# Kernel optimization log

Hardware: AMD Instinct MI355X
Metric: run time of the kernel (lower is better)

## Reference

```python
import jax, jax.numpy as jnp
import numpy as np

B, S, V, D, DV = 8, 2048, 32000, 1024, 1152
NUM_IMG, PATCHES = 4, 576
IMG_POS = [100, 600, 1100, 1600]
IMAGE_TOKEN_ID = 31999


def setup_inputs() -> dict:
    key = jax.random.key(0)
    k1, k2, k3, k4 = jax.random.split(key, 4)
    texts = jax.random.randint(k1, (B, S), 0, 31000)
    texts = texts.at[:, jnp.array(IMG_POS)].set(IMAGE_TOKEN_ID)
    visual_features = jax.random.normal(k2, (B, NUM_IMG * PATCHES, DV), jnp.float32)
    embedding_table = jax.random.normal(k3, (V, D), jnp.float32) * 0.02
    W_proj = jax.random.normal(k4, (DV, D), jnp.float32) * 0.02
    b_proj = jnp.zeros((D,), jnp.float32)
    return {"visual_features": visual_features, "embedding_table": embedding_table,
            "W_proj": W_proj, "b_proj": b_proj, "texts": texts,
            "image_token_id": IMAGE_TOKEN_ID}


def _plan(texts_np, image_token_id, n_visual):
    # Host-side (int-only) plan: per-sample gather indices into [text_emb ; visual]
    # plus the nested block attention mask. Mirrors the torch ragged loops.
    Bn, Sn = texts_np.shape
    idx_list, cid_list, vis_list = [], [], []
    for b in range(Bn):
        pos = np.nonzero(texts_np[b] == image_token_id)[0]
        n = len(pos)
        if n == 0:
            idx_list.append(np.arange(Sn))
            cid_list.append(np.zeros(Sn, np.int64))
            vis_list.append(np.zeros(Sn, bool))
            continue
        per = n_visual // n
        text_chunks = []
        start = 0
        for p in pos:
            if p > start:
                text_chunks.append((start, int(p)))
                start = int(p) + 1
        if start < Sn:
            text_chunks.append((start, Sn))
        idx, cid, vis = [], [], []
        c = 0
        for i in range(n):
            if i < len(text_chunks):
                s, e = text_chunks[i]
                idx.append(np.arange(s, e)); cid.append(np.full(e - s, c)); vis.append(np.zeros(e - s, bool)); c += 1
            idx.append(Sn + np.arange(i * per, (i + 1) * per))
            cid.append(np.full(per, c)); vis.append(np.ones(per, bool)); c += 1
        if n < len(text_chunks):
            s, e = text_chunks[-1]
            idx.append(np.arange(s, e)); cid.append(np.full(e - s, c)); vis.append(np.zeros(e - s, bool))
        idx_list.append(np.concatenate(idx))
        cid_list.append(np.concatenate(cid))
        vis_list.append(np.concatenate(vis))
    L = max(len(x) for x in idx_list)
    idx_p = np.zeros((Bn, L), np.int64)
    valid = np.zeros((Bn, L), np.float32)
    mask = np.zeros((Bn, L, L), np.float32)
    for b in range(Bn):
        l = len(idx_list[b])
        idx_p[b, :l] = idx_list[b]
        valid[b, :l] = 1.0
        cid, vis = cid_list[b], vis_list[b]
        ar = np.arange(l)
        # block-causal: full attention to earlier chunks; within own chunk:
        # visual chunks bidirectional, text chunks causal
        m = (cid[None, :] < cid[:, None]) | (
            (cid[None, :] == cid[:, None]) & (vis[:, None] | (ar[None, :] <= ar[:, None])))
        mask[b, :l, :l] = m.astype(np.float32)
    return idx_p, valid, mask


def reference(visual_features, embedding_table, W_proj, b_proj, texts, image_token_id):
    texts_np = np.asarray(jax.device_get(texts))
    idx, valid, mask = _plan(texts_np, int(image_token_id), visual_features.shape[1])
    projected = visual_features @ W_proj + b_proj          # [B, Nv, D]
    text_emb = embedding_table[texts]                      # [B, S, D]
    combined = jnp.concatenate([text_emb, projected], axis=1)  # [B, S+Nv, D]
    fused = jnp.take_along_axis(combined, jnp.asarray(idx)[:, :, None], axis=1)
    fused = fused * jnp.asarray(valid)[:, :, None]
    return fused, jnp.asarray(mask)[:, None, :, :]
```

## Files before the change

### kernel.cpp

```cpp
#include <hip/hip_runtime.h>
#include <math.h>
#include <stdint.h>

#define MAXI 8
#define MAXSEG (2*MAXI+2)
#define VISBIT (1<<30)

typedef __attribute__((ext_vector_type(8))) short short8;
typedef __attribute__((ext_vector_type(4))) float f32x4;

static __device__ __forceinline__ unsigned short f2bf(float f) {
  union { float f; unsigned int u; } v; v.f = f;
  unsigned int x = v.u;
  unsigned int r = (x + 0x7FFFu + ((x >> 16) & 1u)) >> 16;
  return (unsigned short)r;
}

static __device__ __forceinline__ void gload_lds16(const void* g, void* lds) {
  __builtin_amdgcn_global_load_lds((const __attribute__((address_space(1))) void*)g,
                                   (__attribute__((address_space(3))) void*)lds, 16, 0, 0);
}

__global__ void plan_kernel(const int* __restrict__ texts, const int* __restrict__ imgtok_p,
                            int S, int n_visual, int L,
                            int* __restrict__ seg, int* __restrict__ nsegA, int* __restrict__ lenA,
                            int* __restrict__ perA, int* __restrict__ nimgA, int* __restrict__ ostA)
{
  int b = blockIdx.x;
  __shared__ int spos[256];
  __shared__ int scnt;
  if (threadIdx.x == 0) scnt = 0;
  __syncthreads();
  int tok = imgtok_p[0];
  for (int s = threadIdx.x; s < S; s += blockDim.x) {
    if (texts[(size_t)b*S + s] == tok) {
      int i = atomicAdd(&scnt, 1);
      if (i < 256) spos[i] = s;
    }
  }
  __syncthreads();
  if (threadIdx.x != 0) return;
  int n = scnt; if (n > MAXI) n = MAXI;
  for (int i = 1; i < n; i++) {
    int key = spos[i]; int j = i - 1;
    while (j >= 0 && spos[j] > key) { spos[j+1] = spos[j]; j--; }
    spos[j+1] = key;
  }
  int* sg = seg + b*MAXSEG*4;
  int ns = 0, o = 0, c = 0, per = 1;
  if (n == 0) {
    sg[0] = 0; sg[1] = 0; sg[2] = S; sg[3] = 0; ns = 1; o = S;
  } else {
    per = n_visual / n;
    int tcs[MAXI+1], tce[MAXI+1]; int ntc = 0; int start = 0;
    for (int i = 0; i < n; i++) {
      int p = spos[i];
      if (p > start) { tcs[ntc] = start; tce[ntc] = p; ntc++; }
      start = p + 1;
    }
    if (start < S) { tcs[ntc] = start; tce[ntc] = S; ntc++; }
    for (int i = 0; i < n; i++) {
      if (i < ntc) {
        sg[ns*4+0] = o; sg[ns*4+1] = tcs[i]; sg[ns*4+2] = tce[i]-tcs[i]; sg[ns*4+3] = (c<<1);
        o += tce[i]-tcs[i]; c++; ns++;
      }
      ostA[b*MAXI + i] = o;
      sg[ns*4+0] = o; sg[ns*4+1] = i*per; sg[ns*4+2] = per; sg[ns*4+3] = (c<<1)|1;
      o += per; c++; ns++;
    }
    if (n < ntc) {
      sg[ns*4+0] = o; sg[ns*4+1] = tcs[ntc-1]; sg[ns*4+2] = tce[ntc-1]-tcs[ntc-1]; sg[ns*4+3] = (c<<1);
      o += sg[ns*4+2]; ns++;
    }
  }
  nsegA[b] = ns; lenA[b] = o; perA[b] = per; nimgA[b] = n;
  for (int i = n; i < MAXI; i++) ostA[b*MAXI + i] = 0;
  for (int t = ns; t < MAXSEG; t++) { sg[t*4+0]=0; sg[t*4+1]=0; sg[t*4+2]=0; sg[t*4+3]=0; }
}

__global__ void fill_kernel(const int* __restrict__ texts, int S, int L, int bpb,
                            const int* __restrict__ seg, const int* __restrict__ nsegA,
                            int* __restrict__ srcA, int* __restrict__ cidvA)
{
  int b = blockIdx.x / bpb;
  int j = (blockIdx.x % bpb) * blockDim.x + threadIdx.x;
  if (j >= L) return;
  int ns = nsegA[b];
  const int* sg = seg + b*MAXSEG*4;
  int src = -1, cv = -1;
  for (int t = 0; t < ns; t++) {
    int o = sg[t*4+0], ss = sg[t*4+1], ln = sg[t*4+2], cvis = sg[t*4+3];
    if (j >= o && j < o + ln) {
      if (cvis & 1) src = VISBIT | (ss + (j - o));
      else          src = texts[(size_t)b*S + ss + (j - o)];
      cv = cvis;
    }
  }
  srcA[(size_t)b*L + j] = src;
  cidvA[(size_t)b*L + j] = cv;
}

__global__ void wt_kernel(const float* __restrict__ W, unsigned short* __restrict__ Wt, int D, int DV)
{
  __shared__ float t[32][33];
  int k0 = blockIdx.x*32, n0 = blockIdx.y*32;
  int tx = threadIdx.x, ty = threadIdx.y;
  for (int i = 0; i < 4; i++) {
    int k = k0 + ty + i*8, nn = n0 + tx;
    t[ty+i*8][tx] = (k < DV && nn < D) ? W[(size_t)k*D + nn] : 0.f;
  }
  __syncthreads();
  for (int i = 0; i < 4; i++) {
    int nn = n0 + ty + i*8, k = k0 + tx;
    if (nn < D && k < DV) Wt[(size_t)nn*DV + k] = f2bf(t[tx][ty+i*8]);
  }
}

__global__ void gather_kernel(const float* __restrict__ emb, const int* __restrict__ srcA,
                              float* __restrict__ out, int L, int D)
{
  int bid = blockIdx.x;
  int b = bid / L, j = bid % L;
  int s = srcA[(size_t)b*L + j];
  if (s >= 0 && (s & VISBIT)) return;
  float* orow = out + ((size_t)b*L + j)*(size_t)D;
  if (s < 0) {
    for (int d = threadIdx.x*4; d < D; d += blockDim.x*4)
      *(float4*)&orow[d] = make_float4(0.f,0.f,0.f,0.f);
  } else {
    const float* erow = emb + (size_t)s*D;
    for (int d = threadIdx.x*4; d < D; d += blockDim.x*4)
      *(float4*)&orow[d] = *(const float4*)&erow[d];
  }
}

__launch_bounds__(256)
__global__ void gemm_kernel(const float* __restrict__ vis, const unsigned short* __restrict__ Wt,
                            const float* __restrict__ bproj, float* __restrict__ out,
                            const int* __restrict__ perA, const int* __restrict__ nimgA,
                            const int* __restrict__ ostA,
                            int Nv, int DV, int D, int L, int Mt, int Nt)
{
  __shared__ unsigned short As[128*32];
  __shared__ unsigned short Bs[128*32];
  int bid = blockIdx.x;
  int nt = bid % Nt; int mt = (bid/Nt) % Mt; int b = bid/(Nt*Mt);
  int r0 = mt*128, n0 = nt*128;
  int tid = threadIdx.x; int wv = tid>>6, l = tid&63;
  int wm = wv>>1, wn = wv&1;
  f32x4 acc[4][4];
  for (int m=0;m<4;m++) for (int n=0;n<4;n++) acc[m][n] = (f32x4){0.f,0.f,0.f,0.f};

  int nk = DV/32;
  int lr = l & 15, lk = (l>>4)*8;
  for (int kt = 0; kt < nk; ++kt) {
    int k0 = kt*32;
    for (int q = 0; q < 2; q++) {
      int flat = q*256 + tid;
      int row = flat >> 2, sub = flat & 3;
      const unsigned short* g = Wt + (size_t)(n0+row)*DV + k0 + sub*8;
      gload_lds16(g, (char*)Bs + (size_t)flat*16);
    }
    for (int q = 0; q < 4; q++) {
      int flat = q*256 + tid;
      int row = flat >> 3, ko = (flat & 7)*4;
      int rr = r0 + row; if (rr >= Nv) rr = Nv - 1;
      const float4 v = *(const float4*)(vis + ((size_t)b*Nv + rr)*DV + k0 + ko);
      ushort4 w; w.x = f2bf(v.x); w.y = f2bf(v.y); w.z = f2bf(v.z); w.w = f2bf(v.w);
      *(ushort4*)&As[row*32 + ko] = w;
    }
    __syncthreads();
    short8 av[4], bv[4];
    for (int m = 0; m < 4; m++) av[m] = *(const short8*)&As[(wm*64 + m*16 + lr)*32 + lk];
    for (int n = 0; n < 4; n++) bv[n] = *(const short8*)&Bs[(wn*64 + n*16 + lr)*32 + lk];
    for (int m = 0; m < 4; m++)
      for (int n = 0; n < 4; n++)
        acc[m][n] = __builtin_amdgcn_mfma_f32_16x16x32_bf16(av[m], bv[n], acc[m][n], 0, 0, 0);
    __syncthreads();
  }

  int per = perA[b], nimg = nimgA[b];
  int rmax = nimg * per; if (rmax > Nv) rmax = Nv;
  float bp[4];
  for (int n = 0; n < 4; n++) bp[n] = bproj[n0 + wn*64 + n*16 + lr];
  for (int m = 0; m < 4; m++) {
    for (int rg = 0; rg < 4; rg++) {
      int r = r0 + wm*64 + m*16 + (l>>4)*4 + rg;
      if (r >= rmax) continue;
      int i = r / per, k = r - i*per;
      int j = ostA[b*MAXI + i] + k;
      float* orow = out + ((size_t)b*L + j)*(size_t)D;
      for (int n = 0; n < 4; n++)
        orow[n0 + wn*64 + n*16 + lr] = acc[m][n][rg] + bp[n];
    }
  }
}

static __device__ __forceinline__ float maskval(int ck, int k, int cidq, int visq, int q) {
  int cidk = ck >> 1;
  bool m = (ck >= 0) && ((cidk < cidq) || ((cidk == cidq) && (visq || (k <= q))));
  return m ? 1.f : 0.f;
}

__global__ void mask_kernel(const int* __restrict__ cidvA, float* __restrict__ mask, int L)
{
  int bid = blockIdx.x;
  int b = bid / L, q = bid - b*L;
  const int* crow = cidvA + (size_t)b*L;
  int cq = crow[q];
  float* row = mask + (size_t)bid * (size_t)L;
  bool qvalid = cq >= 0;
  int cidq = cq >> 1, visq = cq & 1;
  if ((L & 3) == 0) {
    for (int k0 = threadIdx.x*4; k0 < L; k0 += blockDim.x*4) {
      float4 o;
      if (!qvalid) {
        o = make_float4(0.f,0.f,0.f,0.f);
      } else {
        int4 ck = *(const int4*)&crow[k0];
        o.x = maskval(ck.x, k0+0, cidq, visq, q);
        o.y = maskval(ck.y, k0+1, cidq, visq, q);
        o.z = maskval(ck.z, k0+2, cidq, visq, q);
        o.w = maskval(ck.w, k0+3, cidq, visq, q);
      }
      *(float4*)&row[k0] = o;
    }
  } else {
    for (int k = threadIdx.x; k < L; k += blockDim.x)
      row[k] = qvalid ? maskval(crow[k], k, cidq, visq, q) : 0.f;
  }
}

extern "C" void kernel_launch(void* const* d_in, const int* in_sizes, int n_in,
                              void* d_out, int out_size, void* d_ws, size_t ws_size,
                              hipStream_t stream)
{
  const float* visf = (const float*)d_in[0];
  const float* emb  = (const float*)d_in[1];
  const float* W    = (const float*)d_in[2];
  const float* bpj  = (const float*)d_in[3];
  const int* texts  = (const int*)d_in[4];
  const int* imgtok = (const int*)d_in[5];

  const int B = 8;
  int D  = in_sizes[3];
  int DV = in_sizes[2] / D;
  int S  = in_sizes[4] / B;
  int Nv = in_sizes[0] / (B * DV);

  double qq = (double)out_size / (double)B;
  int L = (int)((-(double)D + sqrt((double)D*(double)D + 4.0*qq)) * 0.5 + 0.5);

  float* out   = (float*)d_out;
  float* maskp = out + (size_t)B * (size_t)L * (size_t)D;

  char* p = (char*)d_ws;
  int* srcA  = (int*)p; p += (size_t)B*L*4;
  int* cidvA = (int*)p; p += (size_t)B*L*4;
  int* segA  = (int*)p; p += (size_t)B*MAXSEG*4*4;
  int* nsegA = (int*)p; p += B*4;
  int* lenA  = (int*)p; p += B*4;
  int* perA  = (int*)p; p += B*4;
  int* nimgA = (int*)p; p += B*4;
  int* ostA  = (int*)p; p += B*MAXI*4;
  p = (char*)(((uintptr_t)p + 255) & ~(uintptr_t)255);
  unsigned short* Wt = (unsigned short*)p; p += (size_t)D*DV*2;

  plan_kernel<<<B, 256, 0, stream>>>(texts, imgtok, S, Nv, L, segA, nsegA, lenA, perA, nimgA, ostA);
  int bpb = (L + 255) / 256;
  fill_kernel<<<B*bpb, 256, 0, stream>>>(texts, S, L, bpb, segA, nsegA, srcA, cidvA);
  wt_kernel<<<dim3((DV+31)/32, (D+31)/32), dim3(32,8), 0, stream>>>(W, Wt, D, DV);
  gather_kernel<<<B*L, 256, 0, stream>>>(emb, srcA, out, L, D);
  int Mt = (Nv + 127) / 128, Nt = D / 128;
  gemm_kernel<<<B*Mt*Nt, 256, 0, stream>>>(visf, Wt, bpj, out, perA, nimgA, ostA, Nv, DV, D, L, Mt, Nt);
  mask_kernel<<<B*L, 256, 0, stream>>>(cidvA, maskp, L);
}
```

Baseline: 974.0 us.

## Simplify mask to prefix threshold, precast visuals, flatten GEMM across batch

Each mask row is rewritten as a prefix test `k < E`, where `E` is the end of the chunk the query attends to, computed once per query position in the fill kernel. This removes the per-element cid comparisons and the per-key reads in the mask kernel, and each block now writes several rows. Visual features are cast to bf16 in a separate pass so the GEMM can load both operands with direct global-to-LDS loads. The GEMM M dimension is flattened across batches, with an XCD-aware block swizzle and per-row batch decoding in the epilogue. The gather kernel becomes grid-stride. The cost is an extra read-write pass over the visual features and a new dependence on the chunks being contiguous and ordered.

```diff
diff --git a/kernel.cpp b/kernel.cpp
--- a/kernel.cpp
+++ b/kernel.cpp
@@ -80,24 +80,23 @@
 
 __global__ void fill_kernel(const int* __restrict__ texts, int S, int L, int bpb,
                             const int* __restrict__ seg, const int* __restrict__ nsegA,
-                            int* __restrict__ srcA, int* __restrict__ cidvA)
+                            int* __restrict__ srcA, int* __restrict__ EiA)
 {
   int b = blockIdx.x / bpb;
   int j = (blockIdx.x % bpb) * blockDim.x + threadIdx.x;
   if (j >= L) return;
   int ns = nsegA[b];
   const int* sg = seg + b*MAXSEG*4;
-  int src = -1, cv = -1;
+  int src = -1, E = 0;
   for (int t = 0; t < ns; t++) {
     int o = sg[t*4+0], ss = sg[t*4+1], ln = sg[t*4+2], cvis = sg[t*4+3];
     if (j >= o && j < o + ln) {
-      if (cvis & 1) src = VISBIT | (ss + (j - o));
-      else          src = texts[(size_t)b*S + ss + (j - o)];
-      cv = cvis;
+      if (cvis & 1) { src = VISBIT | (ss + (j - o)); E = o + ln; }
+      else          { src = texts[(size_t)b*S + ss + (j - o)]; E = j + 1; }
     }
   }
   srcA[(size_t)b*L + j] = src;
-  cidvA[(size_t)b*L + j] = cv;
+  EiA[(size_t)b*L + j] = E;
 }
 
 __global__ void wt_kernel(const float* __restrict__ W, unsigned short* __restrict__ Wt, int D, int DV)
@@ -116,26 +115,37 @@
   }
 }
 
+__global__ void viscast_kernel(const float* __restrict__ vis, unsigned short* __restrict__ visb, size_t n)
+{
+  size_t i = ((size_t)blockIdx.x*blockDim.x + threadIdx.x)*4;
+  size_t stride = (size_t)gridDim.x*blockDim.x*4;
+  for (; i + 3 < n; i += stride) {
+    float4 v = *(const float4*)(vis + i);
+    ushort4 w; w.x = f2bf(v.x); w.y = f2bf(v.y); w.z = f2bf(v.z); w.w = f2bf(v.w);
+    *(ushort4*)(visb + i) = w;
+  }
+}
+
 __global__ void gather_kernel(const float* __restrict__ emb, const int* __restrict__ srcA,
-                              float* __restrict__ out, int L, int D)
-{
-  int bid = blockIdx.x;
-  int b = bid / L, j = bid % L;
-  int s = srcA[(size_t)b*L + j];
-  if (s >= 0 && (s & VISBIT)) return;
-  float* orow = out + ((size_t)b*L + j)*(size_t)D;
-  if (s < 0) {
-    for (int d = threadIdx.x*4; d < D; d += blockDim.x*4)
-      *(float4*)&orow[d] = make_float4(0.f,0.f,0.f,0.f);
-  } else {
-    const float* erow = emb + (size_t)s*D;
-    for (int d = threadIdx.x*4; d < D; d += blockDim.x*4)
-      *(float4*)&orow[d] = *(const float4*)&erow[d];
+                              float* __restrict__ out, int nrows, int D)
+{
+  for (int j = blockIdx.x; j < nrows; j += gridDim.x) {
+    int s = srcA[j];
+    if (s >= 0 && (s & VISBIT)) continue;
+    float* orow = out + (size_t)j*(size_t)D;
+    if (s < 0) {
+      for (int d = threadIdx.x*4; d < D; d += blockDim.x*4)
+        *(float4*)&orow[d] = make_float4(0.f,0.f,0.f,0.f);
+    } else {
+      const float* erow = emb + (size_t)s*D;
+      for (int d = threadIdx.x*4; d < D; d += blockDim.x*4)
+        *(float4*)&orow[d] = *(const float4*)&erow[d];
+    }
   }
 }
 
 __launch_bounds__(256)
-__global__ void gemm_kernel(const float* __restrict__ vis, const unsigned short* __restrict__ Wt,
+__global__ void gemm_kernel(const unsigned short* __restrict__ visb, const unsigned short* __restrict__ Wt,
                             const float* __restrict__ bproj, float* __restrict__ out,
                             const int* __restrict__ perA, const int* __restrict__ nimgA,
                             const int* __restrict__ ostA,
@@ -143,9 +153,11 @@
 {
   __shared__ unsigned short As[128*32];
   __shared__ unsigned short Bs[128*32];
-  int bid = blockIdx.x;
-  int nt = bid % Nt; int mt = (bid/Nt) % Mt; int b = bid/(Nt*Mt);
-  int r0 = mt*128, n0 = nt*128;
+  int nwg = Mt*Nt;
+  int hw = blockIdx.x;
+  int bid = ((nwg & 7) == 0) ? ((hw & 7)*(nwg>>3) + (hw>>3)) : hw;
+  int nt = bid % Nt; int mt = bid / Nt;
+  int gr0 = mt*128, n0 = nt*128;
   int tid = threadIdx.x; int wv = tid>>6, l = tid&63;
   int wm = wv>>1, wn = wv&1;
   f32x4 acc[4][4];
@@ -158,16 +170,8 @@
     for (int q = 0; q < 2; q++) {
       int flat = q*256 + tid;
       int row = flat >> 2, sub = flat & 3;
-      const unsigned short* g = Wt + (size_t)(n0+row)*DV + k0 + sub*8;
-      gload_lds16(g, (char*)Bs + (size_t)flat*16);
-    }
-    for (int q = 0; q < 4; q++) {
-      int flat = q*256 + tid;
-      int row = flat >> 3, ko = (flat & 7)*4;
-      int rr = r0 + row; if (rr >= Nv) rr = Nv - 1;
-      const float4 v = *(const float4*)(vis + ((size_t)b*Nv + rr)*DV + k0 + ko);
-      ushort4 w; w.x = f2bf(v.x); w.y = f2bf(v.y); w.z = f2bf(v.z); w.w = f2bf(v.w);
-      *(ushort4*)&As[row*32 + ko] = w;
+      gload_lds16(visb + (size_t)(gr0+row)*DV + k0 + sub*8, (char*)As + (size_t)flat*16);
+      gload_lds16(Wt   + (size_t)(n0 +row)*DV + k0 + sub*8, (char*)Bs + (size_t)flat*16);
     }
     __syncthreads();
     short8 av[4], bv[4];
@@ -179,13 +183,14 @@
     __syncthreads();
   }
 
-  int per = perA[b], nimg = nimgA[b];
-  int rmax = nimg * per; if (rmax > Nv) rmax = Nv;
   float bp[4];
   for (int n = 0; n < 4; n++) bp[n] = bproj[n0 + wn*64 + n*16 + lr];
   for (int m = 0; m < 4; m++) {
     for (int rg = 0; rg < 4; rg++) {
-      int r = r0 + wm*64 + m*16 + (l>>4)*4 + rg;
+      int grow = gr0 + wm*64 + m*16 + (l>>4)*4 + rg;
+      int b = grow / Nv, r = grow - b*Nv;
+      int per = perA[b];
+      int rmax = nimgA[b] * per; if (rmax > Nv) rmax = Nv;
       if (r >= rmax) continue;
       int i = r / per, k = r - i*per;
       int j = ostA[b*MAXI + i] + k;
@@ -196,38 +201,34 @@
   }
 }
 
-static __device__ __forceinline__ float maskval(int ck, int k, int cidq, int visq, int q) {
-  int cidk = ck >> 1;
-  bool m = (ck >= 0) && ((cidk < cidq) || ((cidk == cidq) && (visq || (k <= q))));
-  return m ? 1.f : 0.f;
-}
-
-__global__ void mask_kernel(const int* __restrict__ cidvA, float* __restrict__ mask, int L)
-{
-  int bid = blockIdx.x;
-  int b = bid / L, q = bid - b*L;
-  const int* crow = cidvA + (size_t)b*L;
-  int cq = crow[q];
-  float* row = mask + (size_t)bid * (size_t)L;
-  bool qvalid = cq >= 0;
-  int cidq = cq >> 1, visq = cq & 1;
+#define MROWS 4
+__global__ void mask_kernel(const int* __restrict__ EiA, float* __restrict__ mask, int L, int nrows)
+{
+  int g0 = blockIdx.x * MROWS;
   if ((L & 3) == 0) {
-    for (int k0 = threadIdx.x*4; k0 < L; k0 += blockDim.x*4) {
-      float4 o;
-      if (!qvalid) {
-        o = make_float4(0.f,0.f,0.f,0.f);
-      } else {
-        int4 ck = *(const int4*)&crow[k0];
-        o.x = maskval(ck.x, k0+0, cidq, visq, q);
-        o.y = maskval(ck.y, k0+1, cidq, visq, q);
-        o.z = maskval(ck.z, k0+2, cidq, visq, q);
-        o.w = maskval(ck.w, k0+3, cidq, visq, q);
+    for (int rr = 0; rr < MROWS; rr++) {
+      int row = g0 + rr;
+      if (row >= nrows) return;
+      int E = EiA[row];
+      float* rp = mask + (size_t)row * (size_t)L;
+      for (int k0 = threadIdx.x*4; k0 < L; k0 += blockDim.x*4) {
+        float4 o;
+        o.x = (k0+0 < E) ? 1.f : 0.f;
+        o.y = (k0+1 < E) ? 1.f : 0.f;
+        o.z = (k0+2 < E) ? 1.f : 0.f;
+        o.w = (k0+3 < E) ? 1.f : 0.f;
+        *(float4*)&rp[k0] = o;
       }
-      *(float4*)&row[k0] = o;
     }
   } else {
-    for (int k = threadIdx.x; k < L; k += blockDim.x)
-      row[k] = qvalid ? maskval(crow[k], k, cidq, visq, q) : 0.f;
+    for (int rr = 0; rr < MROWS; rr++) {
+      int row = g0 + rr;
+      if (row >= nrows) return;
+      int E = EiA[row];
+      float* rp = mask + (size_t)row * (size_t)L;
+      for (int k = threadIdx.x; k < L; k += blockDim.x)
+        rp[k] = (k < E) ? 1.f : 0.f;
+    }
   }
 }
 
@@ -256,7 +257,7 @@
 
   char* p = (char*)d_ws;
   int* srcA  = (int*)p; p += (size_t)B*L*4;
-  int* cidvA = (int*)p; p += (size_t)B*L*4;
+  int* EiA   = (int*)p; p += (size_t)B*L*4;
   int* segA  = (int*)p; p += (size_t)B*MAXSEG*4*4;
   int* nsegA = (int*)p; p += B*4;
   int* lenA  = (int*)p; p += B*4;
@@ -265,13 +266,17 @@
   int* ostA  = (int*)p; p += B*MAXI*4;
   p = (char*)(((uintptr_t)p + 255) & ~(uintptr_t)255);
   unsigned short* Wt = (unsigned short*)p; p += (size_t)D*DV*2;
+  p = (char*)(((uintptr_t)p + 255) & ~(uintptr_t)255);
+  unsigned short* visb = (unsigned short*)p; p += (size_t)B*Nv*DV*2;
 
   plan_kernel<<<B, 256, 0, stream>>>(texts, imgtok, S, Nv, L, segA, nsegA, lenA, perA, nimgA, ostA);
   int bpb = (L + 255) / 256;
-  fill_kernel<<<B*bpb, 256, 0, stream>>>(texts, S, L, bpb, segA, nsegA, srcA, cidvA);
+  fill_kernel<<<B*bpb, 256, 0, stream>>>(texts, S, L, bpb, segA, nsegA, srcA, EiA);
   wt_kernel<<<dim3((DV+31)/32, (D+31)/32), dim3(32,8), 0, stream>>>(W, Wt, D, DV);
-  gather_kernel<<<B*L, 256, 0, stream>>>(emb, srcA, out, L, D);
-  int Mt = (Nv + 127) / 128, Nt = D / 128;
-  gemm_kernel<<<B*Mt*Nt, 256, 0, stream>>>(visf, Wt, bpj, out, perA, nimgA, ostA, Nv, DV, D, L, Mt, Nt);
-  mask_kernel<<<B*L, 256, 0, stream>>>(cidvA, maskp, L);
-}
+  viscast_kernel<<<2048, 256, 0, stream>>>(visf, visb, (size_t)B*Nv*DV);
+  gather_kernel<<<2048, 256, 0, stream>>>(emb, srcA, out, B*L, D);
+  int Mt = (B*Nv) / 128, Nt = D / 128;
+  if ((B*Nv) % 128 != 0) Mt = (B*Nv + 127)/128;
+  gemm_kernel<<<Mt*Nt, 256, 0, stream>>>(visb, Wt, bpj, out, perA, nimgA, ostA, Nv, DV, D, L, Mt, Nt);
+  mask_kernel<<<(B*L + MROWS-1)/MROWS, 256, 0, stream>>>(EiA, maskp, L, B*L);
+}
```

Result: no change. 955.6 us (-1.9%).
